# Kernel tuning notes

Hardware: AMD Instinct MI355X
Metric: run time of the kernel (lower is better)

## Reference

```python
import jax, jax.numpy as jnp
import numpy as np

N = 40000          # nodes per type (dev, repo)
H, D = 8, 64       # heads, head dim
HID = H * D        # 512 hidden channels
OUT = 256
N_CONVS = 4        # 2 towers (res, link) x 2 layers
EDGE_TYPES = [(0, 1), (1, 0), (0, 0)]  # (src_type, dst_type)
SQRT_D = float(np.sqrt(D))


def _lin(x, w, b):
    return x @ w + b


def _seg_softmax(a, idx, n):
    m = jax.ops.segment_max(a, idx, num_segments=n)
    e = jnp.exp(a - m[idx])
    s = jax.ops.segment_sum(e, idx, num_segments=n)
    return e / (s[idx] + 1e-16)


def _hgt_conv(xs, edges, kw, kb, qw, qb, vw, vb, aw, ab, skip, a_rel, m_rel, p_rel):
    # xs: [x_dev, x_repo] each [N, HID]; edges: list of [2, E]
    k = [_lin(xs[t], kw[t], kb[t]).reshape(-1, H, D) for t in range(2)]
    q = [_lin(xs[t], qw[t], qb[t]).reshape(-1, H, D) for t in range(2)]
    v = [_lin(xs[t], vw[t], vb[t]).reshape(-1, H, D) for t in range(2)]
    out = [jnp.zeros_like(k[0]), jnp.zeros_like(k[1])]
    for r, (st, dt) in enumerate(EDGE_TYPES):
        src, dst = edges[r][0], edges[r][1]
        k_rel = jnp.einsum('nhd,hde->nhe', k[st], a_rel[r])
        v_rel = jnp.einsum('nhd,hde->nhe', v[st], m_rel[r])
        alpha = (q[dt][dst] * k_rel[src]).sum(-1) * p_rel[r] / SQRT_D  # [E, H]
        alpha = _seg_softmax(alpha, dst, N)
        msg = v_rel[src] * alpha[..., None]                            # [E, H, D]
        out[dt] = out[dt] + jax.ops.segment_sum(msg, dst, num_segments=N)
    res = []
    for t in range(2):
        o = _lin(jax.nn.gelu(out[t].reshape(-1, HID), approximate=False), aw[t], ab[t])
        g = jax.nn.sigmoid(skip[t])
        res.append(g * o + (1.0 - g) * xs[t])
    return res


def setup_inputs() -> dict:
    key = jax.random.key(0)
    ks = iter(jax.random.split(key, 48))
    def nrm(shape, scale=1.0):
        return jax.random.normal(next(ks), shape, dtype=jnp.float32) * scale
    E1, E2, E3, EP = 250000, 250000, 150000, 100000
    inp = {}
    inp['x_dev'] = nrm((N, HID))
    inp['x_repo'] = nrm((N, HID))
    inp['ei_dr'] = jax.random.randint(next(ks), (2, E1), 0, N, dtype=jnp.int32)
    inp['ei_rd'] = jax.random.randint(next(ks), (2, E2), 0, N, dtype=jnp.int32)
    inp['ei_dd'] = jax.random.randint(next(ks), (2, E3), 0, N, dtype=jnp.int32)
    inp['pos_edge'] = jax.random.randint(next(ks), (2, EP), 0, N, dtype=jnp.int32)
    inp['neg_edge'] = jax.random.randint(next(ks), (2, EP), 0, N, dtype=jnp.int32)
    s = 1.0 / np.sqrt(HID)
    for nm in ('k', 'q', 'v', 'a'):
        inp[nm + '_w'] = nrm((N_CONVS, 2, HID, HID), s)
        inp[nm + '_b'] = jnp.zeros((N_CONVS, 2, HID), jnp.float32)
    inp['skip'] = jnp.ones((N_CONVS, 2), jnp.float32)
    sd = 1.0 / np.sqrt(D)
    inp['a_rel'] = nrm((N_CONVS, 3, H, D, D), sd)
    inp['m_rel'] = nrm((N_CONVS, 3, H, D, D), sd)
    inp['p_rel'] = jnp.ones((N_CONVS, 3, H), jnp.float32)
    inp['reg_w1'] = nrm((HID, OUT), s); inp['reg_b1'] = jnp.zeros((OUT,), jnp.float32)
    inp['reg_w2'] = nrm((OUT, 1), 1.0 / np.sqrt(OUT)); inp['reg_b2'] = jnp.zeros((1,), jnp.float32)
    inp['src_w'] = nrm((HID, OUT), s); inp['src_b'] = jnp.zeros((OUT,), jnp.float32)
    inp['dst_w'] = nrm((HID, OUT), s); inp['dst_b'] = jnp.zeros((OUT,), jnp.float32)
    inp['fin_w'] = nrm((OUT, 1), 1.0 / np.sqrt(OUT)); inp['fin_b'] = jnp.zeros((1,), jnp.float32)
    return inp


def reference(x_dev, x_repo, ei_dr, ei_rd, ei_dd, pos_edge, neg_edge,
              k_w, k_b, q_w, q_b, v_w, v_b, a_w, a_b, skip,
              a_rel, m_rel, p_rel,
              reg_w1, reg_b1, reg_w2, reg_b2,
              src_w, src_b, dst_w, dst_b, fin_w, fin_b):
    edges = [ei_dr, ei_rd, ei_dd]

    def embed(conv_ids):
        xs = [x_dev, x_repo]
        for c in conv_ids:
            xs = _hgt_conv(xs, edges, k_w[c], k_b[c], q_w[c], q_b[c], v_w[c], v_b[c],
                           a_w[c], a_b[c], skip[c], a_rel[c], m_rel[c], p_rel[c])
            xs = [jax.nn.leaky_relu(x, 0.01) for x in xs]
        return xs

    res = embed([0, 1])   # embedding_res tower
    lnk = embed([2, 3])   # embedding_link tower
    emb_dev = res[0] + lnk[0]
    emb_repo = res[1] + lnk[1]

    fit_dev = _lin(_lin(emb_dev, reg_w1, reg_b1), reg_w2, reg_b2).squeeze(-1)
    fit_repo = _lin(_lin(emb_repo, reg_w1, reg_b1), reg_w2, reg_b2).squeeze(-1)

    def link(zs, zd):
        h = _lin(zs, src_w, src_b) * _lin(zd, dst_w, dst_b)
        return jax.nn.sigmoid(_lin(h, fin_w, fin_b)).squeeze(-1)

    pos = link(emb_dev[pos_edge[0]], emb_repo[pos_edge[1]])
    neg = link(emb_dev[neg_edge[0]], emb_repo[neg_edge[1]])
    score = jnp.concatenate([pos, neg], axis=0)
    return (fit_dev, fit_repo, score)
```

## Files before the change

kernel.cpp:

```cpp
#include <hip/hip_runtime.h>
#include <math.h>

#define NNODES 40000
#define NB ((size_t)20480000)
#define RPS 40004

typedef __attribute__((ext_vector_type(8))) short bf16x8;
typedef __attribute__((ext_vector_type(4))) float f32x4;

__device__ __forceinline__ ushort f2bf(float f) {
  unsigned u = __float_as_uint(f);
  u += 0x7FFFu + ((u >> 16) & 1u);
  return (ushort)(u >> 16);
}
__device__ __forceinline__ float b2f(ushort h) {
  return __uint_as_float((unsigned)h << 16);
}
__device__ __forceinline__ float gelu_f(float x) {
  return 0.5f * x * (1.0f + erff(x * 0.70710678118654752440f));
}

__device__ __forceinline__ void gll16(const ushort* g, ushort* l) {
  __builtin_amdgcn_global_load_lds(
      (const __attribute__((address_space(1))) unsigned int*)(const void*)g,
      (__attribute__((address_space(3))) unsigned int*)(void*)l, 16, 0, 0);
}

template<int EPI>
__global__ __launch_bounds__(256)
void gemm_bf16_kernel(const ushort* __restrict__ Av, const ushort* __restrict__ Bt,
                      const float* __restrict__ bias,
                      ushort* __restrict__ C0, ushort* __restrict__ C1,
                      int M, int PW,
                      const ushort* __restrict__ xprev, const float* __restrict__ skipv,
                      int nwgx)
{
  const int K = 512;
  __shared__ char smem[32768];
  ushort* Sm = (ushort*)smem;
  float*  Es = (float*)smem;

  const int nwg = (int)gridDim.x;
  const int q8 = nwg >> 3, r8 = nwg & 7;
  const int xcd = (int)blockIdx.x & 7, i8 = (int)blockIdx.x >> 3;
  const int logical = (xcd < r8 ? xcd * (q8 + 1) : r8 * (q8 + 1) + (xcd - r8) * q8) + i8;
  const int bm = (logical / nwgx) * 128;
  const int bnl = (logical % nwgx) * 128;
  const int pan = (bnl >= PW) ? 1 : 0;
  const int bn = bnl - pan * PW;
  ushort* __restrict__ C = pan ? C1 : C0;

  const int tid = threadIdx.x, lane = tid & 63, wave = tid >> 6;
  const int wr = (wave >> 1) * 64, wc = (wave & 1) * 64;
  const int fr = lane & 15, fq = lane >> 4;
  f32x4 acc[4][4] = {};

  const int rdsw = (fq ^ ((fr >> 1) & 3)) * 8;
  const int csrc = ((lane & 3) ^ ((lane >> 3) & 3)) * 8;
  const int r0 = wave * 32 + (lane >> 2);
  int ra0 = bm + r0;      if (ra0 >= M) ra0 = M - 1;
  int ra1 = bm + r0 + 16; if (ra1 >= M) ra1 = M - 1;
  const ushort* ga0 = Av + (size_t)ra0 * K + csrc;
  const ushort* ga1 = Av + (size_t)ra1 * K + csrc;
  const ushort* gb0 = Bt + (size_t)(bnl + r0) * K + csrc;
  const ushort* gb1 = Bt + (size_t)(bnl + r0 + 16) * K + csrc;
  ushort* la0[2] = {Sm + wave * 1024,        Sm + 8192 + wave * 1024};
  ushort* la1[2] = {la0[0] + 512,            la0[1] + 512};
  ushort* lb0[2] = {Sm + 4096 + wave * 1024, Sm + 12288 + wave * 1024};
  ushort* lb1[2] = {lb0[0] + 512,            lb0[1] + 512};

  gll16(ga0, la0[0]); gll16(ga1, la1[0]); gll16(gb0, lb0[0]); gll16(gb1, lb1[0]);
  ga0 += 32; ga1 += 32; gb0 += 32; gb1 += 32;
  __syncthreads();

  #pragma unroll 4
  for (int it = 0; it < 16; ++it) {
    const int cur = it & 1;
    if (it < 15) {
      gll16(ga0, la0[cur ^ 1]); gll16(ga1, la1[cur ^ 1]);
      gll16(gb0, lb0[cur ^ 1]); gll16(gb1, lb1[cur ^ 1]);
      ga0 += 32; ga1 += 32; gb0 += 32; gb1 += 32;
    }
    const ushort* Ab = Sm + cur * 8192;
    const ushort* Bb = Ab + 4096;
    bf16x8 af[4], bfv[4];
    #pragma unroll
    for (int i = 0; i < 4; ++i) {
      af[i]  = *(const bf16x8*)&Ab[(wr + i * 16 + fr) * 32 + rdsw];
      bfv[i] = *(const bf16x8*)&Bb[(wc + i * 16 + fr) * 32 + rdsw];
    }
    #pragma unroll
    for (int mi = 0; mi < 4; ++mi)
      #pragma unroll
      for (int ni = 0; ni < 4; ++ni)
        acc[mi][ni] = __builtin_amdgcn_mfma_f32_16x16x32_bf16(af[mi], bfv[ni], acc[mi][ni], 0, 0, 0);
    __syncthreads();
  }

  float gate = 0.f, og = 0.f;
  if (EPI == 2) { gate = 1.f / (1.f + __expf(-skipv[0])); og = 1.f - gate; }
  #pragma unroll
  for (int qr = 0; qr < 4; ++qr) {
    __syncthreads();
    #pragma unroll
    for (int mi = 0; mi < 4; ++mi) {
      if (((wr + mi * 16) >> 5) != qr) continue;
      const int lr = ((wr + mi * 16) & 31) + fq * 4;
      #pragma unroll
      for (int ni = 0; ni < 4; ++ni) {
        const int col = wc + ni * 16 + fr;
        #pragma unroll
        for (int r = 0; r < 4; ++r)
          Es[(lr + r) * 132 + col] = acc[mi][ni][r];
      }
    }
    __syncthreads();
    const int lrow = tid >> 3;
    const int c0 = (tid & 7) * 16;
    const int grow = bm + qr * 32 + lrow;
    if (grow < M) {
      float v[16];
      #pragma unroll
      for (int j = 0; j < 4; ++j)
        *(float4*)&v[j * 4] = *(const float4*)&Es[lrow * 132 + c0 + j * 4];
      if (EPI == 1 || EPI == 2) {
        #pragma unroll
        for (int j = 0; j < 4; ++j) {
          float4 b4 = *(const float4*)(bias + bnl + c0 + j * 4);
          v[j*4] += b4.x; v[j*4+1] += b4.y; v[j*4+2] += b4.z; v[j*4+3] += b4.w;
        }
      }
      size_t base = (size_t)grow * PW + bn + c0;
      if (EPI == 2) {
        uint4 x0 = *(const uint4*)(xprev + base);
        uint4 x1 = *(const uint4*)(xprev + base + 8);
        #pragma unroll
        for (int j = 0; j < 8; ++j) {
          unsigned w = (j < 4) ? ((const unsigned*)&x0)[j] : ((const unsigned*)&x1)[j - 4];
          float a  = gate * v[2*j]   + og * __uint_as_float(w << 16);
          float bq = gate * v[2*j+1] + og * __uint_as_float(w & 0xFFFF0000u);
          v[2*j]   = a  > 0.f ? a  : 0.01f * a;
          v[2*j+1] = bq > 0.f ? bq : 0.01f * bq;
        }
      }
      if (EPI == 4) {
        uint4 x0 = *(const uint4*)(C + base);
        uint4 x1 = *(const uint4*)(C + base + 8);
        #pragma unroll
        for (int j = 0; j < 8; ++j) {
          unsigned w = (j < 4) ? ((const unsigned*)&x0)[j] : ((const unsigned*)&x1)[j - 4];
          v[2*j]   += __uint_as_float(w << 16);
          v[2*j+1] += __uint_as_float(w & 0xFFFF0000u);
        }
      }
      ushort ob[16];
      #pragma unroll
      for (int j = 0; j < 16; ++j) ob[j] = f2bf(v[j]);
      *(uint4*)(C + base)     = *(uint4*)&ob[0];
      *(uint4*)(C + base + 8) = *(uint4*)&ob[8];
    }
  }
}

__global__ __launch_bounds__(256)
void transpose_w_batch(const float* __restrict__ q_w, const float* __restrict__ a_w,
                       const float* __restrict__ src_w, const float* __restrict__ dst_w,
                       ushort* __restrict__ wqT, ushort* __restrict__ waT,
                       ushort* __restrict__ srcwT, ushort* __restrict__ dstwT)
{
  const int z = blockIdx.z;
  const float* W; ushort* Wt; int N;
  if (z < 8)       { W = q_w + (size_t)z * 262144;       Wt = wqT + (size_t)z * 262144;       N = 512; }
  else if (z < 16) { W = a_w + (size_t)(z - 8) * 262144; Wt = waT + (size_t)(z - 8) * 262144; N = 512; }
  else if (z == 16){ W = src_w; Wt = srcwT; N = 256; }
  else             { W = dst_w; Wt = dstwT; N = 256; }
  int bn = blockIdx.x * 32, bk = blockIdx.y * 32;
  if (bn >= N) return;
  __shared__ float t[32][33];
  int x = threadIdx.x & 31, y = threadIdx.x >> 5;
  #pragma unroll
  for (int yy = y; yy < 32; yy += 8) t[yy][x] = W[(size_t)(bk + yy) * N + bn + x];
  __syncthreads();
  #pragma unroll
  for (int yy = y; yy < 32; yy += 8) Wt[(size_t)(bn + yy) * 512 + bk + x] = f2bf(t[x][yy]);
}

__global__ __launch_bounds__(256)
void fold_rel_batch(const float* __restrict__ k_w, const float* __restrict__ k_b,
                    const float* __restrict__ v_w, const float* __restrict__ v_b,
                    const float* __restrict__ a_rel, const float* __restrict__ m_rel,
                    ushort* __restrict__ wkvT, float* __restrict__ bfuse)
{
  const int z = blockIdx.z;
  const int kv = z / 12, i = z % 12;
  const int c = i / 3, r = i % 3;
  const int st_tab[3] = {0, 1, 0};
  const int stp = st_tab[r];
  const float* Win  = (kv ? v_w : k_w) + (size_t)(c * 2 + stp) * 262144;
  const float* bin  = (kv ? v_b : k_b) + (size_t)(c * 2 + stp) * 512;
  const float* Arel = (kv ? m_rel : a_rel) + (size_t)i * 32768;
  ushort* W2t = wkvT + (size_t)i * 524288 + (size_t)kv * 262144;
  float*  b2  = bfuse + i * 1024 + kv * 512;

  const int h = blockIdx.x;
  __shared__ float Al[4096];
  for (int j = threadIdx.x; j < 4096; j += 256) Al[j] = Arel[(size_t)h * 4096 + j];
  __syncthreads();
  const int wv = threadIdx.x >> 6, lane = threadIdx.x & 63;
  for (int rr = 0; rr < 16; ++rr) {
    int row = blockIdx.y * 64 + wv * 16 + rr;
    if (row > 512) continue;
    const float* src = (row < 512) ? (Win + (size_t)row * 512 + h * 64) : (bin + h * 64);
    float acc = 0.f;
    #pragma unroll
    for (int d = 0; d < 64; ++d) acc = fmaf(src[d], Al[d * 64 + lane], acc);
    if (row < 512) W2t[(size_t)(h * 64 + lane) * 512 + row] = f2bf(acc);
    else           b2[h * 64 + lane] = acc;
  }
}

__global__ __launch_bounds__(256)
void make_wfit_kernel(const float* __restrict__ w1, const float* __restrict__ b1,
                      const float* __restrict__ w2, const float* __restrict__ b2,
                      float* __restrict__ wfit)
{
  for (int k = threadIdx.x; k < 512; k += 256) {
    float acc = 0.f;
    for (int j = 0; j < 256; ++j) acc = fmaf(w1[(size_t)k * 256 + j], w2[j], acc);
    wfit[k] = acc;
  }
  if (threadIdx.x == 0) {
    float acc = 0.f;
    for (int j = 0; j < 256; ++j) acc = fmaf(b1[j], w2[j], acc);
    wfit[512] = acc + b2[0];
  }
}

__global__ __launch_bounds__(256)
void hist_batch(const int* __restrict__ d0, const int* __restrict__ d1,
                const int* __restrict__ d2, unsigned* __restrict__ cnt3)
{
  const int z = blockIdx.z;
  const int* dst = (z == 0) ? d0 : (z == 1) ? d1 : d2;
  const int E = (z == 2) ? 150000 : 250000;
  unsigned* cnt = cnt3 + (size_t)z * NNODES;
  for (int i = blockIdx.x * 256 + threadIdx.x; i < E; i += gridDim.x * 256)
    atomicAdd(&cnt[dst[i]], 1u);
}

__global__ __launch_bounds__(256)
void scan_batch(const unsigned* __restrict__ cnt3, unsigned* __restrict__ rowptr3,
                unsigned* __restrict__ woff3)
{
  const int z = blockIdx.x;
  const unsigned* cnt = cnt3 + (size_t)z * NNODES;
  unsigned* rowptr = rowptr3 + (size_t)z * RPS;
  unsigned* woff   = woff3 + (size_t)z * NNODES;
  __shared__ unsigned csum[256];
  const int t = threadIdx.x;
  const int lo = t * 160, hi = (lo + 160 < NNODES) ? lo + 160 : NNODES;
  unsigned s = 0;
  for (int i = lo; i < hi; i += 4) {
    uint4 v = *(const uint4*)&cnt[i];
    s += v.x + v.y + v.z + v.w;
  }
  csum[t] = s;
  __syncthreads();
  if (t == 0) {
    unsigned run = 0;
    for (int j = 0; j < 256; ++j) { unsigned v = csum[j]; csum[j] = run; run += v; }
    rowptr[NNODES] = run;
  }
  __syncthreads();
  unsigned run = csum[t];
  for (int i = lo; i < hi; i += 4) {
    uint4 cv = *(const uint4*)&cnt[i];
    uint4 rp;
    rp.x = run; run += cv.x;
    rp.y = run; run += cv.y;
    rp.z = run; run += cv.z;
    rp.w = run; run += cv.w;
    *(uint4*)&rowptr[i] = rp;
    *(uint4*)&woff[i]   = rp;
  }
}

__global__ __launch_bounds__(256)
void fill_batch(const int* __restrict__ d0, const int* __restrict__ d1,
                const int* __restrict__ d2, unsigned* __restrict__ woff3,
                unsigned* __restrict__ order)
{
  const int z = blockIdx.z;
  const int* dst = (z == 0) ? d0 : (z == 1) ? d1 : d2;
  const int E = (z == 2) ? 150000 : 250000;
  unsigned* woff = woff3 + (size_t)z * NNODES;
  unsigned* ord  = order + ((z == 0) ? 0 : (z == 1) ? 250000 : 500000);
  for (int i = blockIdx.x * 256 + threadIdx.x; i < E; i += gridDim.x * 256) {
    unsigned slot = atomicAdd(&woff[dst[i]], 1u);
    ord[slot] = (unsigned)i;
  }
}

__global__ __launch_bounds__(256)
void edge_softmax_kernel(const ushort* __restrict__ q, const ushort* __restrict__ kr,
                         const int* __restrict__ srcp,
                         const unsigned* __restrict__ rowptr, const unsigned* __restrict__ order,
                         const float* __restrict__ prel, float* __restrict__ alpha)
{
  int d = (int)((blockIdx.x * 256u + threadIdx.x) >> 6);
  int lane = threadIdx.x & 63;
  if (d >= NNODES) return;
  unsigned start = rowptr[d], end = rowptr[d + 1];
  if (start == end) return;
  const int h = lane >> 3;
  const float pscale = prel[h] * 0.125f;

  uint4 qv = *(const uint4*)(q + (size_t)d * 512 + lane * 8);
  const unsigned* pq = (const unsigned*)&qv;
  float qf[8];
  #pragma unroll
  for (int j = 0; j < 4; ++j) {
    qf[2*j]   = __uint_as_float(pq[j] << 16);
    qf[2*j+1] = __uint_as_float(pq[j] & 0xFFFF0000u);
  }

  float m = -3e38f;
  for (unsigned idx = start; idx < end; ++idx) {
    int e = (int)order[idx];
    int s = srcp[e];
    uint4 kv = *(const uint4*)(kr + (size_t)s * 512 + lane * 8);
    const unsigned* pk = (const unsigned*)&kv;
    float acc = 0.f;
    #pragma unroll
    for (int j = 0; j < 4; ++j) {
      acc = fmaf(qf[2*j],   __uint_as_float(pk[j] << 16),         acc);
      acc = fmaf(qf[2*j+1], __uint_as_float(pk[j] & 0xFFFF0000u), acc);
    }
    acc += __shfl_xor(acc, 1);
    acc += __shfl_xor(acc, 2);
    acc += __shfl_xor(acc, 4);
    float a = acc * pscale;
    if ((lane & 7) == 0) alpha[(size_t)idx * 8 + h] = a;
    m = fmaxf(m, a);
  }
  asm volatile("s_waitcnt vmcnt(0)" ::: "memory");
  float ssum = 0.f;
  if ((lane & 7) == 0) {
    for (unsigned idx = start; idx < end; ++idx) {
      float ev = __expf(alpha[(size_t)idx * 8 + h] - m);
      alpha[(size_t)idx * 8 + h] = ev;
      ssum += ev;
    }
  }
  asm volatile("s_waitcnt vmcnt(0)" ::: "memory");
  if ((lane & 7) == 0) {
    float rs = 1.f / (ssum + 1e-16f);
    for (unsigned idx = start; idx < end; ++idx)
      alpha[(size_t)idx * 8 + h] *= rs;
  }
}

template<int ACCUM, int GELU>
__global__ __launch_bounds__(256)
void gather_msg_kernel(const float* __restrict__ alpha, const ushort* __restrict__ vrel,
                       const int* __restrict__ srcp,
                       const unsigned* __restrict__ rowptr, const unsigned* __restrict__ order,
                       const ushort* __restrict__ accin, ushort* __restrict__ outp)
{
  int d = (int)((blockIdx.x * 256u + threadIdx.x) >> 6);
  int lane = threadIdx.x & 63;
  if (d >= NNODES) return;
  unsigned start = rowptr[d], end = rowptr[d + 1];
  const int h = lane >> 3;
  float acc[8] = {};
  for (unsigned idx = start; idx < end; ++idx) {
    int e = (int)order[idx];
    int s = srcp[e];
    float w = alpha[(size_t)idx * 8 + h];
    uint4 vv = *(const uint4*)(vrel + (size_t)s * 512 + lane * 8);
    const unsigned* pv = (const unsigned*)&vv;
    #pragma unroll
    for (int j = 0; j < 4; ++j) {
      acc[2*j]   = fmaf(__uint_as_float(pv[j] << 16),         w, acc[2*j]);
      acc[2*j+1] = fmaf(__uint_as_float(pv[j] & 0xFFFF0000u), w, acc[2*j+1]);
    }
  }
  if (ACCUM) {
    uint4 old = *(const uint4*)(accin + (size_t)d * 512 + lane * 8);
    const unsigned* po = (const unsigned*)&old;
    #pragma unroll
    for (int j = 0; j < 4; ++j) {
      acc[2*j]   += __uint_as_float(po[j] << 16);
      acc[2*j+1] += __uint_as_float(po[j] & 0xFFFF0000u);
    }
  }
  ushort t[8];
  #pragma unroll
  for (int j = 0; j < 8; ++j) t[j] = f2bf(GELU ? gelu_f(acc[j]) : acc[j]);
  *(uint4*)(outp + (size_t)d * 512 + lane * 8) = *(uint4*)t;
}

template<int MODE>
__global__ __launch_bounds__(256)
void fitdot_kernel(const ushort* __restrict__ cur, const float* __restrict__ wfit,
                   float* __restrict__ out, int M)
{
  int row = (int)((blockIdx.x * 256u + threadIdx.x) >> 6);
  int lane = threadIdx.x & 63;
  if (row >= M) return;
  uint4 v = *(const uint4*)(cur + (size_t)row * 512 + lane * 8);
  const unsigned* pv = (const unsigned*)&v;
  float wreg[8];
  *(float4*)wreg       = *(const float4*)(wfit + lane * 8);
  *(float4*)(wreg + 4) = *(const float4*)(wfit + lane * 8 + 4);
  float acc = 0.f;
  #pragma unroll
  for (int j = 0; j < 4; ++j) {
    acc = fmaf(__uint_as_float(pv[j] << 16),         wreg[2 * j],     acc);
    acc = fmaf(__uint_as_float(pv[j] & 0xFFFF0000u), wreg[2 * j + 1], acc);
  }
  #pragma unroll
  for (int off = 1; off < 64; off <<= 1) acc += __shfl_xor(acc, off);
  if (lane == 0) {
    if (MODE == 0) out[row] = acc;
    else           out[row] += acc + wfit[512];
  }
}

__global__ __launch_bounds__(256)
void link_score_kernel(const ushort* __restrict__ se, const ushort* __restrict__ de,
                       const float* __restrict__ sb, const float* __restrict__ db,
                       const int* __restrict__ si, const int* __restrict__ di,
                       int E, const float* __restrict__ fw, const float* __restrict__ fb,
                       float* __restrict__ out)
{
  int wv = (int)((blockIdx.x * 256u + threadIdx.x) >> 6);
  int lane = threadIdx.x & 63;
  if (wv >= E) return;
  int s = si[wv], d = di[wv];
  ushort4 a = *(const ushort4*)(se + (size_t)s * 256 + lane * 4);
  ushort4 b = *(const ushort4*)(de + (size_t)d * 256 + lane * 4);
  float4 s4 = *(const float4*)(sb + lane * 4);
  float4 d4 = *(const float4*)(db + lane * 4);
  float4 w4 = *(const float4*)(fw + lane * 4);
  float acc = (b2f(a.x) + s4.x) * (b2f(b.x) + d4.x) * w4.x
            + (b2f(a.y) + s4.y) * (b2f(b.y) + d4.y) * w4.y
            + (b2f(a.z) + s4.z) * (b2f(b.z) + d4.z) * w4.z
            + (b2f(a.w) + s4.w) * (b2f(b.w) + d4.w) * w4.w;
  #pragma unroll
  for (int off = 1; off < 64; off <<= 1) acc += __shfl_xor(acc, off);
  if (lane == 0) out[wv] = 1.f / (1.f + __expf(-(acc + fb[0])));
}

__global__ __launch_bounds__(256)
void f32_to_bf16_kernel(const float* __restrict__ in, ushort* __restrict__ out, int n4)
{
  for (int i = blockIdx.x * 256 + threadIdx.x; i < n4; i += gridDim.x * 256) {
    float4 v = ((const float4*)in)[i];
    ushort4 o; o.x = f2bf(v.x); o.y = f2bf(v.y); o.z = f2bf(v.z); o.w = f2bf(v.w);
    ((ushort4*)out)[i] = o;
  }
}

__global__ void diag_kernel(float* __restrict__ out, float v)
{
  if (threadIdx.x == 0 && blockIdx.x == 0) out[0] = v;
}

extern "C" void kernel_launch(void* const* d_in, const int* in_sizes, int n_in,
                              void* d_out, int out_size, void* d_ws, size_t ws_size,
                              hipStream_t stream)
{
  const float* x_dev  = (const float*)d_in[0];
  const float* x_repo = (const float*)d_in[1];
  const int* ei[3] = {(const int*)d_in[2], (const int*)d_in[3], (const int*)d_in[4]};
  const int  Ecnt[3] = {250000, 250000, 150000};
  const int* pos_e = (const int*)d_in[5];
  const int* neg_e = (const int*)d_in[6];
  const float* k_w = (const float*)d_in[7];  const float* k_b = (const float*)d_in[8];
  const float* q_w = (const float*)d_in[9];  const float* q_b = (const float*)d_in[10];
  const float* v_w = (const float*)d_in[11]; const float* v_b = (const float*)d_in[12];
  const float* a_w = (const float*)d_in[13]; const float* a_b = (const float*)d_in[14];
  const float* skip  = (const float*)d_in[15];
  const float* a_rel = (const float*)d_in[16];
  const float* m_rel = (const float*)d_in[17];
  const float* p_rel = (const float*)d_in[18];
  const float* reg_w1 = (const float*)d_in[19]; const float* reg_b1 = (const float*)d_in[20];
  const float* reg_w2 = (const float*)d_in[21]; const float* reg_b2 = (const float*)d_in[22];
  const float* src_w  = (const float*)d_in[23]; const float* src_b  = (const float*)d_in[24];
  const float* dst_w  = (const float*)d_in[25]; const float* dst_b  = (const float*)d_in[26];
  const float* fin_w  = (const float*)d_in[27]; const float* fin_b  = (const float*)d_in[28];
  float* out = (float*)d_out;

  const size_t SE = (size_t)NNODES * 256;
  const size_t tail_bytes =
      2000000ull * 4
    + (size_t)8 * 262144 * 2
    + (size_t)8 * 262144 * 2
    + (size_t)12 * 524288 * 2
    + 131072ull * 2 * 2
    + 12288ull * 4
    + 516ull * 4
    + (size_t)3 * RPS * 4
    + 650000ull * 4
    + (size_t)3 * NNODES * 4 * 2;
  const size_t need_fused  = (6 * NB + 2 * SE) * 2 + tail_bytes;
  const size_t need_nofuse = (5 * NB + 2 * SE) * 2 + tail_bytes;
  int FUSED;
  if      (ws_size >= need_fused)  FUSED = 1;
  else if (ws_size >= need_nofuse) FUSED = 0;
  else {
    diag_kernel<<<1, 64, 0, stream>>>(out, 1000.0f + (float)(ws_size / 1000000));
    return;
  }

  ushort* st   = (ushort*)d_ws;
  ushort* cur0 = st;
  ushort* cur1 = st + NB;
  ushort* S1   = st + 2 * NB;
  ushort* S2   = st + 3 * NB;
  ushort* msgB = st + 4 * NB;
  ushort* S3   = FUSED ? (st + 5 * NB) : S2;
  ushort* se   = st + (FUSED ? 6 : 5) * NB;
  ushort* de   = se + SE;
  float*  alpha = (float*)(de + SE);
  ushort* wqT   = (ushort*)(alpha + 2000000);
  ushort* waT   = wqT + (size_t)8 * 262144;
  ushort* wkvT  = waT + (size_t)8 * 262144;
  ushort* srcwT = wkvT + (size_t)12 * 524288;
  ushort* dstwT = srcwT + 131072;
  float*  bfuse = (float*)(dstwT + 131072);
  float*  wfit  = bfuse + 12288;
  unsigned* rowptr3 = (unsigned*)(wfit + 516);
  unsigned* order   = rowptr3 + (size_t)3 * RPS;
  unsigned* cnt3    = order + 650000;
  unsigned* woff3   = cnt3 + (size_t)3 * NNODES;
  const size_t ord_off[3] = {0, 250000, 500000};

  transpose_w_batch<<<dim3(16, 16, 18), 256, 0, stream>>>(q_w, a_w, src_w, dst_w,
                                                          wqT, waT, srcwT, dstwT);
  fold_rel_batch<<<dim3(8, 9, 24), 256, 0, stream>>>(k_w, k_b, v_w, v_b, a_rel, m_rel,
                                                     wkvT, bfuse);
  make_wfit_kernel<<<1, 256, 0, stream>>>(reg_w1, reg_b1, reg_w2, reg_b2, wfit);
  hipMemsetAsync(cnt3, 0, (size_t)3 * NNODES * 4, stream);
  hist_batch<<<dim3(977, 1, 3), 256, 0, stream>>>(ei[0] + Ecnt[0], ei[1] + Ecnt[1],
                                                  ei[2] + Ecnt[2], cnt3);
  scan_batch<<<3, 256, 0, stream>>>(cnt3, rowptr3, woff3);
  fill_batch<<<dim3(977, 1, 3), 256, 0, stream>>>(ei[0] + Ecnt[0], ei[1] + Ecnt[1],
                                                  ei[2] + Ecnt[2], woff3, order);

  auto gemmQ = [&](const ushort* A, int t, ushort* C) {
    gemm_bf16_kernel<1><<<1252, 256, 0, stream>>>(A, wqT + (size_t)t * 262144,
        q_b + (size_t)t * 512, C, C, NNODES, 512, nullptr, nullptr, 4);
  };
  auto gemmKV = [&](int i, const ushort* A) {
    gemm_bf16_kernel<1><<<2504, 256, 0, stream>>>(A, wkvT + (size_t)i * 524288,
        bfuse + (size_t)i * 1024, S2, S3, NNODES, 512, nullptr, nullptr, 8);
  };
  auto gemmK = [&](int i, const ushort* A) {
    gemm_bf16_kernel<1><<<1252, 256, 0, stream>>>(A, wkvT + (size_t)i * 524288,
        bfuse + (size_t)i * 1024, S2, S2, NNODES, 512, nullptr, nullptr, 4);
  };
  auto gemmV = [&](int i, const ushort* A) {
    gemm_bf16_kernel<1><<<1252, 256, 0, stream>>>(A, wkvT + (size_t)i * 524288 + 262144,
        bfuse + (size_t)i * 1024 + 512, S2, S2, NNODES, 512, nullptr, nullptr, 4);
  };
  auto gemmA = [&](int t, ushort* curb) {
    gemm_bf16_kernel<2><<<1252, 256, 0, stream>>>(S1, waT + (size_t)t * 262144,
        a_b + (size_t)t * 512, curb, curb, NNODES, 512, curb, skip + t, 4);
  };

  auto esm = [&](int c, int r, const ushort* qp) {
    edge_softmax_kernel<<<10000, 256, 0, stream>>>(
        qp, S2, ei[r], rowptr3 + (size_t)r * RPS, order + ord_off[r],
        p_rel + (size_t)(c * 3 + r) * 8, alpha);
  };
  auto gath = [&](int r, int accum, int gelu, const ushort* vrel, ushort* outp) {
    const unsigned* rp = rowptr3 + (size_t)r * RPS;
    const unsigned* od = order + ord_off[r];
    if (accum) {
      if (gelu) gather_msg_kernel<1, 1><<<10000, 256, 0, stream>>>(alpha, vrel, ei[r], rp, od, msgB, outp);
      else      gather_msg_kernel<1, 0><<<10000, 256, 0, stream>>>(alpha, vrel, ei[r], rp, od, msgB, outp);
    } else {
      if (gelu) gather_msg_kernel<0, 1><<<10000, 256, 0, stream>>>(alpha, vrel, ei[r], rp, od, nullptr, outp);
      else      gather_msg_kernel<0, 0><<<10000, 256, 0, stream>>>(alpha, vrel, ei[r], rp, od, nullptr, outp);
    }
  };

  auto run_conv = [&](int c) {
    const int t0 = c * 2, t1 = c * 2 + 1;
    gemmQ(cur0, t0, S1);
    if (FUSED) { gemmKV(c * 3 + 1, cur1); esm(c, 1, S1); }
    else       { gemmK(c * 3 + 1, cur1); esm(c, 1, S1); gemmV(c * 3 + 1, cur1); }
    gath(1, 0, 0, S3, msgB);
    if (FUSED) { gemmKV(c * 3 + 2, cur0); esm(c, 2, S1); }
    else       { gemmK(c * 3 + 2, cur0); esm(c, 2, S1); gemmV(c * 3 + 2, cur0); }
    gath(2, 1, 1, S3, S1);
    if (FUSED) { gemmKV(c * 3 + 0, cur0); gemmQ(cur1, t1, msgB); esm(c, 0, msgB); }
    else       { gemmK(c * 3 + 0, cur0); gemmQ(cur1, t1, msgB); esm(c, 0, msgB);
                 gemmV(c * 3 + 0, cur0); }
    gemmA(t0, cur0);
    gath(0, 0, 1, S3, S1);
    gemmA(t1, cur1);
  };

  f32_to_bf16_kernel<<<2048, 256, 0, stream>>>(x_dev,  cur0, (int)(NB / 4));
  f32_to_bf16_kernel<<<2048, 256, 0, stream>>>(x_repo, cur1, (int)(NB / 4));
  run_conv(0);
  run_conv(1);
  fitdot_kernel<0><<<10000, 256, 0, stream>>>(cur0, wfit, out, NNODES);
  fitdot_kernel<0><<<10000, 256, 0, stream>>>(cur1, wfit, out + NNODES, NNODES);
  gemm_bf16_kernel<3><<<626, 256, 0, stream>>>(cur0, srcwT, nullptr, se, se, NNODES, 256, nullptr, nullptr, 2);
  gemm_bf16_kernel<3><<<626, 256, 0, stream>>>(cur1, dstwT, nullptr, de, de, NNODES, 256, nullptr, nullptr, 2);

  f32_to_bf16_kernel<<<2048, 256, 0, stream>>>(x_dev,  cur0, (int)(NB / 4));
  f32_to_bf16_kernel<<<2048, 256, 0, stream>>>(x_repo, cur1, (int)(NB / 4));
  run_conv(2);
  run_conv(3);
  fitdot_kernel<1><<<10000, 256, 0, stream>>>(cur0, wfit, out, NNODES);
  fitdot_kernel<1><<<10000, 256, 0, stream>>>(cur1, wfit, out + NNODES, NNODES);
  gemm_bf16_kernel<4><<<626, 256, 0, stream>>>(cur0, srcwT, nullptr, se, se, NNODES, 256, nullptr, nullptr, 2);
  gemm_bf16_kernel<4><<<626, 256, 0, stream>>>(cur1, dstwT, nullptr, de, de, NNODES, 256, nullptr, nullptr, 2);

  link_score_kernel<<<25000, 256, 0, stream>>>(se, de, src_b, dst_b, pos_e, pos_e + 100000,
                                               100000, fin_w, fin_b, out + 80000);
  link_score_kernel<<<25000, 256, 0, stream>>>(se, de, src_b, dst_b, neg_e, neg_e + 100000,
                                               100000, fin_w, fin_b, out + 180000);
}
```

Baseline: 3.325 ms.

## Deepen GEMM prefetch pipeline, tile fold_rel via LDS, defer softmax normalization to gather

The GEMM main loop now issues the next-next K tile's async LDS loads right after fragments are read. It waits with vmcnt counters and raw barriers instead of a full __syncthreads per iteration, to overlap global loads with MFMA work. fold_rel_batch stages a 64x64 weight tile in padded shared memory and writes coalesced transposed output, with the bias row handled separately. The edge softmax no longer does a second pass rescaling alpha; it stores per-node reciprocal sums, which the gather kernel multiplies in. This adds a small buffer and relies on hand-placed waitcnt ordering being correct.

```diff
diff --git a/kernel.cpp b/kernel.cpp
--- a/kernel.cpp
+++ b/kernel.cpp
@@ -71,16 +71,15 @@
 
   gll16(ga0, la0[0]); gll16(ga1, la1[0]); gll16(gb0, lb0[0]); gll16(gb1, lb1[0]);
   ga0 += 32; ga1 += 32; gb0 += 32; gb1 += 32;
-  __syncthreads();
-
-  #pragma unroll 4
+  gll16(ga0, la0[1]); gll16(ga1, la1[1]); gll16(gb0, lb0[1]); gll16(gb1, lb1[1]);
+  ga0 += 32; ga1 += 32; gb0 += 32; gb1 += 32;
+
+  #pragma unroll
   for (int it = 0; it < 16; ++it) {
     const int cur = it & 1;
-    if (it < 15) {
-      gll16(ga0, la0[cur ^ 1]); gll16(ga1, la1[cur ^ 1]);
-      gll16(gb0, lb0[cur ^ 1]); gll16(gb1, lb1[cur ^ 1]);
-      ga0 += 32; ga1 += 32; gb0 += 32; gb1 += 32;
-    }
+    if (it < 15) asm volatile("s_waitcnt vmcnt(4)" ::: "memory");
+    else         asm volatile("s_waitcnt vmcnt(0)" ::: "memory");
+    __builtin_amdgcn_s_barrier();
     const ushort* Ab = Sm + cur * 8192;
     const ushort* Bb = Ab + 4096;
     bf16x8 af[4], bfv[4];
@@ -88,14 +87,20 @@
     for (int i = 0; i < 4; ++i) {
       af[i]  = *(const bf16x8*)&Ab[(wr + i * 16 + fr) * 32 + rdsw];
       bfv[i] = *(const bf16x8*)&Bb[(wc + i * 16 + fr) * 32 + rdsw];
+    }
+    asm volatile("s_waitcnt lgkmcnt(0)" ::: "memory");
+    __builtin_amdgcn_s_barrier();
+    if (it < 14) {
+      gll16(ga0, la0[cur]); gll16(ga1, la1[cur]); gll16(gb0, lb0[cur]); gll16(gb1, lb1[cur]);
+      ga0 += 32; ga1 += 32; gb0 += 32; gb1 += 32;
     }
     #pragma unroll
     for (int mi = 0; mi < 4; ++mi)
       #pragma unroll
       for (int ni = 0; ni < 4; ++ni)
         acc[mi][ni] = __builtin_amdgcn_mfma_f32_16x16x32_bf16(af[mi], bfv[ni], acc[mi][ni], 0, 0, 0);
-    __syncthreads();
-  }
+  }
+  __syncthreads();
 
   float gate = 0.f, og = 0.f;
   if (EPI == 2) { gate = 1.f / (1.f + __expf(-skipv[0])); og = 1.f - gate; }
@@ -201,21 +206,33 @@
   const float* Arel = (kv ? m_rel : a_rel) + (size_t)i * 32768;
   ushort* W2t = wkvT + (size_t)i * 524288 + (size_t)kv * 262144;
   float*  b2  = bfuse + i * 1024 + kv * 512;
-
-  const int h = blockIdx.x;
+  const int h = blockIdx.x, kc = blockIdx.y;
+
+  __shared__ float Wl[64][65];
   __shared__ float Al[4096];
   for (int j = threadIdx.x; j < 4096; j += 256) Al[j] = Arel[(size_t)h * 4096 + j];
+  {
+    const int kk = threadIdx.x >> 2, d0 = (threadIdx.x & 3) * 16;
+    const float* src = Win + (size_t)(kc * 64 + kk) * 512 + h * 64 + d0;
+    #pragma unroll
+    for (int j = 0; j < 4; ++j)
+      *(float4*)&Wl[kk][d0 + j * 4] = *(const float4*)(src + j * 4);
+  }
   __syncthreads();
-  const int wv = threadIdx.x >> 6, lane = threadIdx.x & 63;
+  const int wave = threadIdx.x >> 6, lane = threadIdx.x & 63;
+  #pragma unroll 4
   for (int rr = 0; rr < 16; ++rr) {
-    int row = blockIdx.y * 64 + wv * 16 + rr;
-    if (row > 512) continue;
-    const float* src = (row < 512) ? (Win + (size_t)row * 512 + h * 64) : (bin + h * 64);
+    const int e = wave * 16 + rr;
     float acc = 0.f;
     #pragma unroll
-    for (int d = 0; d < 64; ++d) acc = fmaf(src[d], Al[d * 64 + lane], acc);
-    if (row < 512) W2t[(size_t)(h * 64 + lane) * 512 + row] = f2bf(acc);
-    else           b2[h * 64 + lane] = acc;
+    for (int d = 0; d < 64; ++d) acc = fmaf(Wl[lane][d], Al[d * 64 + e], acc);
+    W2t[(size_t)(h * 64 + e) * 512 + kc * 64 + lane] = f2bf(acc);
+  }
+  if (kc == 0 && wave == 0) {
+    float acc = 0.f;
+    #pragma unroll
+    for (int d = 0; d < 64; ++d) acc = fmaf(bin[h * 64 + d], Al[d * 64 + lane], acc);
+    b2[h * 64 + lane] = acc;
   }
 }
 
@@ -305,7 +322,8 @@
 void edge_softmax_kernel(const ushort* __restrict__ q, const ushort* __restrict__ kr,
                          const int* __restrict__ srcp,
                          const unsigned* __restrict__ rowptr, const unsigned* __restrict__ order,
-                         const float* __restrict__ prel, float* __restrict__ alpha)
+                         const float* __restrict__ prel, float* __restrict__ alpha,
+                         float* __restrict__ ssumA)
 {
   int d = (int)((blockIdx.x * 256u + threadIdx.x) >> 6);
   int lane = threadIdx.x & 63;
@@ -344,26 +362,21 @@
     m = fmaxf(m, a);
   }
   asm volatile("s_waitcnt vmcnt(0)" ::: "memory");
-  float ssum = 0.f;
   if ((lane & 7) == 0) {
+    float ssum = 0.f;
     for (unsigned idx = start; idx < end; ++idx) {
       float ev = __expf(alpha[(size_t)idx * 8 + h] - m);
       alpha[(size_t)idx * 8 + h] = ev;
       ssum += ev;
     }
-  }
-  asm volatile("s_waitcnt vmcnt(0)" ::: "memory");
-  if ((lane & 7) == 0) {
-    float rs = 1.f / (ssum + 1e-16f);
-    for (unsigned idx = start; idx < end; ++idx)
-      alpha[(size_t)idx * 8 + h] *= rs;
+    ssumA[(size_t)d * 8 + h] = 1.f / (ssum + 1e-16f);
   }
 }
 
 template<int ACCUM, int GELU>
 __global__ __launch_bounds__(256)
-void gather_msg_kernel(const float* __restrict__ alpha, const ushort* __restrict__ vrel,
-                       const int* __restrict__ srcp,
+void gather_msg_kernel(const float* __restrict__ alpha, const float* __restrict__ ssumA,
+                       const ushort* __restrict__ vrel, const int* __restrict__ srcp,
                        const unsigned* __restrict__ rowptr, const unsigned* __restrict__ order,
                        const ushort* __restrict__ accin, ushort* __restrict__ outp)
 {
@@ -372,11 +385,12 @@
   if (d >= NNODES) return;
   unsigned start = rowptr[d], end = rowptr[d + 1];
   const int h = lane >> 3;
+  const float rs = ssumA[(size_t)d * 8 + h];
   float acc[8] = {};
   for (unsigned idx = start; idx < end; ++idx) {
     int e = (int)order[idx];
     int s = srcp[e];
-    float w = alpha[(size_t)idx * 8 + h];
+    float w = alpha[(size_t)idx * 8 + h] * rs;
     uint4 vv = *(const uint4*)(vrel + (size_t)s * 512 + lane * 8);
     const unsigned* pv = (const unsigned*)&vv;
     #pragma unroll
@@ -503,7 +517,8 @@
     + 516ull * 4
     + (size_t)3 * RPS * 4
     + 650000ull * 4
-    + (size_t)3 * NNODES * 4 * 2;
+    + (size_t)3 * NNODES * 4 * 2
+    + 320000ull * 4;
   const size_t need_fused  = (6 * NB + 2 * SE) * 2 + tail_bytes;
   const size_t need_nofuse = (5 * NB + 2 * SE) * 2 + tail_bytes;
   int FUSED;
@@ -535,11 +550,12 @@
   unsigned* order   = rowptr3 + (size_t)3 * RPS;
   unsigned* cnt3    = order + 650000;
   unsigned* woff3   = cnt3 + (size_t)3 * NNODES;
+  float*    ssumA   = (float*)(woff3 + (size_t)3 * NNODES);
   const size_t ord_off[3] = {0, 250000, 500000};
 
   transpose_w_batch<<<dim3(16, 16, 18), 256, 0, stream>>>(q_w, a_w, src_w, dst_w,
                                                           wqT, waT, srcwT, dstwT);
-  fold_rel_batch<<<dim3(8, 9, 24), 256, 0, stream>>>(k_w, k_b, v_w, v_b, a_rel, m_rel,
+  fold_rel_batch<<<dim3(8, 8, 24), 256, 0, stream>>>(k_w, k_b, v_w, v_b, a_rel, m_rel,
                                                      wkvT, bfuse);
   make_wfit_kernel<<<1, 256, 0, stream>>>(reg_w1, reg_b1, reg_w2, reg_b2, wfit);
   hipMemsetAsync(cnt3, 0, (size_t)3 * NNODES * 4, stream);
@@ -573,17 +589,17 @@
   auto esm = [&](int c, int r, const ushort* qp) {
     edge_softmax_kernel<<<10000, 256, 0, stream>>>(
         qp, S2, ei[r], rowptr3 + (size_t)r * RPS, order + ord_off[r],
-        p_rel + (size_t)(c * 3 + r) * 8, alpha);
+        p_rel + (size_t)(c * 3 + r) * 8, alpha, ssumA);
   };
   auto gath = [&](int r, int accum, int gelu, const ushort* vrel, ushort* outp) {
     const unsigned* rp = rowptr3 + (size_t)r * RPS;
     const unsigned* od = order + ord_off[r];
     if (accum) {
-      if (gelu) gather_msg_kernel<1, 1><<<10000, 256, 0, stream>>>(alpha, vrel, ei[r], rp, od, msgB, outp);
-      else      gather_msg_kernel<1, 0><<<10000, 256, 0, stream>>>(alpha, vrel, ei[r], rp, od, msgB, outp);
+      if (gelu) gather_msg_kernel<1, 1><<<10000, 256, 0, stream>>>(alpha, ssumA, vrel, ei[r], rp, od, msgB, outp);
+      else      gather_msg_kernel<1, 0><<<10000, 256, 0, stream>>>(alpha, ssumA, vrel, ei[r], rp, od, msgB, outp);
     } else {
-      if (gelu) gather_msg_kernel<0, 1><<<10000, 256, 0, stream>>>(alpha, vrel, ei[r], rp, od, nullptr, outp);
-      else      gather_msg_kernel<0, 0><<<10000, 256, 0, stream>>>(alpha, vrel, ei[r], rp, od, nullptr, outp);
+      if (gelu) gather_msg_kernel<0, 1><<<10000, 256, 0, stream>>>(alpha, ssumA, vrel, ei[r], rp, od, nullptr, outp);
+      else      gather_msg_kernel<0, 0><<<10000, 256, 0, stream>>>(alpha, ssumA, vrel, ei[r], rp, od, nullptr, outp);
     }
   };
 
```

Result: faster. 3.222 ms (-3.1%).
